# Kernel tuning notes

Hardware: AMD Instinct MI355X
Metric: run time of the kernel (lower is better)

The kernel has to match this reference:

```python
import jax, jax.numpy as jnp
import numpy as np

N, E = 50000, 800000
F_IN, HID, HEADS, NCLS, EF = 16, 32, 4, 5, 8
HC = HID * HEADS
NEG_SLOPE = 0.2


def segment_softmax(scores, seg, num_segments):
    # scores: [E,H], seg: [E] destination node ids
    m = jax.ops.segment_max(scores, seg, num_segments=num_segments)
    e = jnp.exp(scores - m[seg])
    s = jax.ops.segment_sum(e, seg, num_segments=num_segments)
    return e / (s[seg] + 1e-16)


def gat_conv(x, edge_index, edge_attr, W, We, att_src, att_dst, att_edge, bias):
    # PyG GATConv, concat=True, edge_dim=HEADS, eval mode (no dropout)
    n = x.shape[0]
    src, dst = edge_index[0], edge_index[1]
    xp = (x @ W.T).reshape(n, HEADS, HID)                 # [N,H,C]
    a_src = jnp.einsum('nhc,hc->nh', xp, att_src)          # [N,H]
    a_dst = jnp.einsum('nhc,hc->nh', xp, att_dst)
    ep = (edge_attr @ We.T).reshape(-1, HEADS, HID)        # [E,H,C]
    a_e = jnp.einsum('ehc,hc->eh', ep, att_edge)
    alpha = jax.nn.leaky_relu(a_src[src] + a_dst[dst] + a_e, NEG_SLOPE)
    alpha = segment_softmax(alpha, dst, n)                 # softmax over in-edges of dst
    out = jax.ops.segment_sum(xp[src] * alpha[:, :, None], dst, num_segments=n)
    return out.reshape(n, HC) + bias


def setup_inputs() -> dict:
    key = jax.random.key(0)
    ks = jax.random.split(key, 24)
    p = lambda k, shp: (jax.random.normal(k, shp, dtype=jnp.float32) * 0.1)
    inp = {
        'x': jax.random.normal(ks[0], (N, F_IN), dtype=jnp.float32),
        'edge_index': jax.random.randint(ks[1], (2, E), 0, N, dtype=jnp.int64),
        'edge_attr': jax.random.normal(ks[2], (E, EF), dtype=jnp.float32),
        # edge encoder: Linear(EF,HID) -> relu -> Linear(HID,HEADS)
        'ee_w1': p(ks[3], (HID, EF)), 'ee_b1': jnp.zeros((HID,), jnp.float32),
        'ee_w2': p(ks[4], (HEADS, HID)), 'ee_b2': jnp.zeros((HEADS,), jnp.float32),
        # GATConv 1: in=F_IN
        'g1_W': p(ks[5], (HC, F_IN)), 'g1_We': p(ks[6], (HC, HEADS)),
        'g1_as': p(ks[7], (HEADS, HID)), 'g1_ad': p(ks[8], (HEADS, HID)),
        'g1_ae': p(ks[9], (HEADS, HID)), 'g1_b': jnp.zeros((HC,), jnp.float32),
        # GATConv 2: in=HC
        'g2_W': p(ks[10], (HC, HC)), 'g2_We': p(ks[11], (HC, HEADS)),
        'g2_as': p(ks[12], (HEADS, HID)), 'g2_ad': p(ks[13], (HEADS, HID)),
        'g2_ae': p(ks[14], (HEADS, HID)), 'g2_b': jnp.zeros((HC,), jnp.float32),
        # skip projection and classifier
        'skip_w': p(ks[15], (HC, F_IN)), 'skip_b': jnp.zeros((HC,), jnp.float32),
        'cls_w': p(ks[16], (NCLS, HC)), 'cls_b': jnp.zeros((NCLS,), jnp.float32),
    }
    return inp


def reference(x, edge_index, edge_attr, ee_w1, ee_b1, ee_w2, ee_b2,
              g1_W, g1_We, g1_as, g1_ad, g1_ae, g1_b,
              g2_W, g2_We, g2_as, g2_ad, g2_ae, g2_b,
              skip_w, skip_b, cls_w, cls_b):
    ea = jax.nn.relu(edge_attr @ ee_w1.T + ee_b1) @ ee_w2.T + ee_b2   # [E,HEADS]
    skip = x @ skip_w.T + skip_b                                       # [N,HC]
    h = jax.nn.elu(gat_conv(x, edge_index, ea, g1_W, g1_We, g1_as, g1_ad, g1_ae, g1_b))
    h = jax.nn.elu(gat_conv(h, edge_index, ea, g2_W, g2_We, g2_as, g2_ad, g2_ae, g2_b))
    h = h + skip
    return h @ cls_w.T + cls_b                                          # logits [N,NCLS]
```

## Files before the change

### kernel.cpp

```cpp
#include <hip/hip_runtime.h>
#include <hip/hip_bf16.h>
#include <math.h>

#define NN 50000
#define EE 800000
#define F_IN 16
#define HID 32
#define HEADS 4
#define HC 128
#define NCLS 5
#define EF 8
#define NEG_SLOPE 0.2f
#define SCAN_BLOCKS 196
#define NB_NODE 1024
#define NB_EDGE (EE/256)
#define POISON 0xAAAAAAAAu

typedef __attribute__((ext_vector_type(8))) short short8;
typedef __attribute__((ext_vector_type(4))) float floatx4;
typedef __attribute__((ext_vector_type(2))) float floatx2;

__device__ __forceinline__ float lrelu_f(float v) { return v > 0.f ? v : NEG_SLOPE * v; }
__device__ __forceinline__ float elu_f(float v) { return v > 0.f ? v : expm1f(v); }
__device__ __forceinline__ floatx2 splat2(float v) { floatx2 r; r.x = v; r.y = v; return r; }
__device__ __forceinline__ unsigned short f2bf(float v) {
  __hip_bfloat16 b = __float2bfloat16(v);
  unsigned short u; __builtin_memcpy(&u, &b, 2); return u;
}
__device__ __forceinline__ float bf2f(unsigned short u) {
  unsigned v = (unsigned)u << 16; float f; __builtin_memcpy(&f, &v, 4); return f;
}
__device__ __forceinline__ unsigned short pk2_fp8(float a, float b) {
  return (unsigned short)__builtin_amdgcn_cvt_pk_fp8_f32(a, b, 0, false);
}
__device__ __forceinline__ unsigned char pk1_fp8(float a) {
  return (unsigned char)__builtin_amdgcn_cvt_pk_fp8_f32(a, a, 0, false);
}
__device__ __forceinline__ floatx2 unpk_fp8(unsigned short u) {
  return __builtin_amdgcn_cvt_pk_f32_fp8((unsigned)u, false);
}
__device__ __forceinline__ int pk4_fp8(float a, float b, float c, float d) {
  int w = __builtin_amdgcn_cvt_pk_fp8_f32(a, b, 0, false);
  w = __builtin_amdgcn_cvt_pk_fp8_f32(c, d, w, true);
  return w;
}
__device__ __forceinline__ int pk2bf(float a, float b) {
  return (int)((unsigned)f2bf(a) | ((unsigned)f2bf(b) << 16));
}

__global__ void __launch_bounds__(256) k_hist(const int* __restrict__ ei, int* __restrict__ counts,
                                              int* __restrict__ rank) {
  int e = blockIdx.x*256 + threadIdx.x;
  if (e >= EE) return;
  unsigned ret = (unsigned)atomicAdd(&counts[ei[EE + e]], 1);
  rank[e] = (int)(ret - POISON);
}

__global__ void __launch_bounds__(256) k_scan_block(const int* __restrict__ counts, int* __restrict__ bsum) {
  __shared__ int s[256];
  int tid = threadIdx.x;
  int idx = blockIdx.x*256 + tid;
  s[tid] = (idx < NN) ? (int)((unsigned)counts[idx] - POISON) : 0;
  for (int o = 128; o; o >>= 1) { __syncthreads(); if (tid < o) s[tid] += s[tid + o]; }
  if (tid == 0) bsum[blockIdx.x] = s[0];
}

__global__ void __launch_bounds__(256) k_scan_top(const int* __restrict__ bsum, int* __restrict__ bexcl,
                                                  int* __restrict__ row_start,
                                                  const float* __restrict__ clw, const float* __restrict__ skw,
                                                  const float* __restrict__ skb, const float* __restrict__ clb,
                                                  const float* __restrict__ We1, const float* __restrict__ ae1,
                                                  const float* __restrict__ We2, const float* __restrict__ ae2,
                                                  float* __restrict__ mcls, float* __restrict__ cb2,
                                                  float* __restrict__ sve_g) {
  __shared__ int s[256];
  int tid = threadIdx.x;
  int v = (tid < SCAN_BLOCKS) ? bsum[tid] : 0;
  s[tid] = v; __syncthreads();
  for (int o = 1; o < 256; o <<= 1) {
    int t2 = (tid >= o) ? s[tid - o] : 0;
    __syncthreads();
    s[tid] += t2;
    __syncthreads();
  }
  if (tid < SCAN_BLOCKS) bexcl[tid] = s[tid] - v;
  if (tid == 0) row_start[NN] = EE;
  if (tid < NCLS*F_IN) {
    int k = tid >> 4, f = tid & 15;
    float acc = 0.f;
    for (int c = 0; c < HC; ++c) acc = fmaf(clw[k*HC + c], skw[c*F_IN + f], acc);
    mcls[tid] = acc;
  } else if (tid < NCLS*F_IN + NCLS) {
    int k = tid - NCLS*F_IN;
    float acc = clb[k];
    for (int c = 0; c < HC; ++c) acc = fmaf(clw[k*HC + c], skb[c], acc);
    cb2[k] = acc;
  } else if (tid < NCLS*F_IN + NCLS + 32) {
    int t2 = tid - (NCLS*F_IN + NCLS);
    int layer = t2 >> 4, idx = t2 & 15, k = idx >> 2, h = idx & 3;
    const float* We = layer ? We2 : We1;
    const float* ae = layer ? ae2 : ae1;
    float s2 = 0.f;
    for (int c = 0; c < HID; ++c) s2 += We[(h*HID + c)*HEADS + k] * ae[h*HID + c];
    sve_g[layer*16 + k*4 + h] = s2;
  }
}

__global__ void __launch_bounds__(256) k_scan_final(const int* __restrict__ counts, const int* __restrict__ bexcl,
                                                    int* __restrict__ row_start) {
  __shared__ int s[256];
  int tid = threadIdx.x;
  int idx = blockIdx.x*256 + tid;
  int v = (idx < NN) ? (int)((unsigned)counts[idx] - POISON) : 0;
  s[tid] = v; __syncthreads();
  for (int o = 1; o < 256; o <<= 1) {
    int t2 = (tid >= o) ? s[tid - o] : 0;
    __syncthreads();
    s[tid] += t2;
    __syncthreads();
  }
  int excl = s[tid] - v + bexcl[blockIdx.x];
  if (idx < NN) row_start[idx] = excl;
}

__global__ void __launch_bounds__(256) k_fused(
    const float* __restrict__ x, const float* __restrict__ W,
    const float* __restrict__ as_, const float* __restrict__ ad_,
    const float* __restrict__ g2w, unsigned short* __restrict__ w2b,
    unsigned short* __restrict__ xp8u, float* __restrict__ a_src, float* __restrict__ a_dst,
    const float* __restrict__ eattr, const float* __restrict__ w1, const float* __restrict__ b1,
    const float* __restrict__ w2, const float* __restrict__ b2,
    const float* __restrict__ sve_g,
    const int* __restrict__ ei, const int* __restrict__ rank, const int* __restrict__ row_start,
    int4* __restrict__ erec) {
  int tid = threadIdx.x;
  if (blockIdx.x < NB_NODE) {
    __shared__ float sW[HC*17];
    __shared__ float sas[HC], sad[HC];
    __shared__ float sxw[4][16];
    int nb = blockIdx.x;
    if (nb < (HC*HC)/256) w2b[nb*256 + tid] = f2bf(g2w[nb*256 + tid]);
    for (int i = tid; i < HC*F_IN; i += 256) { int r = i >> 4, k = i & 15; sW[r*17 + k] = W[i]; }
    if (tid < HC) { sas[tid] = as_[tid]; sad[tid] = ad_[tid]; }
    __syncthreads();
    int wv = tid >> 6, lane = tid & 63;
    for (int base = nb*4; base < NN; base += NB_NODE*4) {
      int n = base + wv;
      if (n >= NN) continue;
      if (lane < 16) sxw[wv][lane] = x[(size_t)n*F_IN + lane];
      float xv0 = 0.f, xv1 = 0.f;
      #pragma unroll
      for (int k = 0; k < F_IN; ++k) {
        float xk = sxw[wv][k];
        xv0 = fmaf(xk, sW[lane*17 + k], xv0);
        xv1 = fmaf(xk, sW[(lane + 64)*17 + k], xv1);
      }
      float xo0 = __shfl_xor(xv0, 1), xo1 = __shfl_xor(xv1, 1);
      if (!(lane & 1)) {
        xp8u[(size_t)n*64 + (lane >> 1)]      = pk2_fp8(xv0, xo0);
        xp8u[(size_t)n*64 + 32 + (lane >> 1)] = pk2_fp8(xv1, xo1);
      }
      float vs0 = xv0 * sas[lane],      vd0 = xv0 * sad[lane];
      float vs1 = xv1 * sas[lane + 64], vd1 = xv1 * sad[lane + 64];
      #pragma unroll
      for (int m = 16; m; m >>= 1) {
        vs0 += __shfl_xor(vs0, m); vd0 += __shfl_xor(vd0, m);
        vs1 += __shfl_xor(vs1, m); vd1 += __shfl_xor(vd1, m);
      }
      if ((lane & 31) == 0) {
        int hh = lane >> 5;
        a_src[n*HEADS + hh]     = vs0; a_dst[n*HEADS + hh]     = vd0;
        a_src[n*HEADS + 2 + hh] = vs1; a_dst[n*HEADS + 2 + hh] = vd1;
      }
    }
    return;
  }
  int e = (blockIdx.x - NB_NODE)*256 + tid;
  if (e >= EE) return;
  int src = ei[e], dst = ei[EE + e];
  int pos = row_start[dst] + rank[e];
  const float4* ap = (const float4*)(eattr + (size_t)e*EF);
  float4 A0 = ap[0], A1 = ap[1];
  float ea0=A0.x, ea1=A0.y, ea2=A0.z, ea3=A0.w, ea4=A1.x, ea5=A1.y, ea6=A1.z, ea7=A1.w;
  float enc0=b2[0], enc1=b2[1], enc2=b2[2], enc3=b2[3];
  #pragma unroll
  for (int j = 0; j < HID; ++j) {
    float hsum = b1[j];
    hsum = fmaf(ea0, w1[j*EF+0], hsum); hsum = fmaf(ea1, w1[j*EF+1], hsum);
    hsum = fmaf(ea2, w1[j*EF+2], hsum); hsum = fmaf(ea3, w1[j*EF+3], hsum);
    hsum = fmaf(ea4, w1[j*EF+4], hsum); hsum = fmaf(ea5, w1[j*EF+5], hsum);
    hsum = fmaf(ea6, w1[j*EF+6], hsum); hsum = fmaf(ea7, w1[j*EF+7], hsum);
    hsum = fmaxf(hsum, 0.f);
    enc0 = fmaf(hsum, w2[0*HID+j], enc0);
    enc1 = fmaf(hsum, w2[1*HID+j], enc1);
    enc2 = fmaf(hsum, w2[2*HID+j], enc2);
    enc3 = fmaf(hsum, w2[3*HID+j], enc3);
  }
  float ae1_0 = enc0*sve_g[0]  + enc1*sve_g[4]  + enc2*sve_g[8]   + enc3*sve_g[12];
  float ae1_1 = enc0*sve_g[1]  + enc1*sve_g[5]  + enc2*sve_g[9]   + enc3*sve_g[13];
  float ae1_2 = enc0*sve_g[2]  + enc1*sve_g[6]  + enc2*sve_g[10]  + enc3*sve_g[14];
  float ae1_3 = enc0*sve_g[3]  + enc1*sve_g[7]  + enc2*sve_g[11]  + enc3*sve_g[15];
  float ae2_0 = enc0*sve_g[16] + enc1*sve_g[20] + enc2*sve_g[24]  + enc3*sve_g[28];
  float ae2_1 = enc0*sve_g[17] + enc1*sve_g[21] + enc2*sve_g[25]  + enc3*sve_g[29];
  float ae2_2 = enc0*sve_g[18] + enc1*sve_g[22] + enc2*sve_g[26]  + enc3*sve_g[30];
  float ae2_3 = enc0*sve_g[19] + enc1*sve_g[23] + enc2*sve_g[27]  + enc3*sve_g[31];
  int4 r;
  r.x = src;
  r.y = pk2bf(ae1_0, ae1_1);
  r.z = pk2bf(ae1_2, ae1_3);
  r.w = pk4_fp8(ae2_0, ae2_1, ae2_2, ae2_3);
  erec[pos] = r;
}

__global__ void __launch_bounds__(256) k_agg1xp2(
    const int* __restrict__ row_start, const int4* __restrict__ erec,
    const unsigned short* __restrict__ xp8u,
    const float4* __restrict__ a_srcv, const float4* __restrict__ a_dstv,
    const float* __restrict__ bias,
    const unsigned short* __restrict__ w2b,
    const float* __restrict__ as2, const float* __restrict__ ad2,
    unsigned char* __restrict__ xp8u2, float* __restrict__ a_src2, float* __restrict__ a_dst2) {
  __shared__ float4 sew[4][64];
  __shared__ unsigned short h1s[16][136];
  int wv = threadIdx.x >> 6, lane = threadIdx.x & 63;
  int h = lane >> 4, c2 = lane*2;
  for (int i = 0; i < 4; ++i) {
    int n = blockIdx.x*16 + wv*4 + i;
    int beg = row_start[n], end = row_start[n+1];
    float4 ad4 = a_dstv[n];
    floatx2 accA = {0.f, 0.f}, accB = {0.f, 0.f};
    float ssum = 0.f;
    for (int cb = beg; cb < end; cb += 64) {
      int cnt = end - cb; if (cnt > 64) cnt = 64;
      int le = lane < cnt ? lane : cnt - 1;
      int4 rc = erec[cb + le];
      int sl = rc.x;
      float4 as4 = a_srcv[sl];
      float ae0 = bf2f((unsigned short)((unsigned)rc.y & 0xffffu));
      float ae1 = bf2f((unsigned short)((unsigned)rc.y >> 16));
      float ae2 = bf2f((unsigned short)((unsigned)rc.z & 0xffffu));
      float ae3 = bf2f((unsigned short)((unsigned)rc.z >> 16));
      float4 wf;
      wf.x = __expf(lrelu_f(as4.x + ad4.x + ae0));
      wf.y = __expf(lrelu_f(as4.y + ad4.y + ae1));
      wf.z = __expf(lrelu_f(as4.z + ad4.z + ae2));
      wf.w = __expf(lrelu_f(as4.w + ad4.w + ae3));
      if (lane >= cnt) { wf.x = 0.f; wf.y = 0.f; wf.z = 0.f; wf.w = 0.f; }
      sew[wv][lane] = wf;
      const float* ewp = (const float*)(&sew[wv][0]);
      int ng = (cnt + 7) >> 3;
      for (int g = 0; g < ng; ++g) {
        int j8 = g << 3;
        int s0 = __builtin_amdgcn_readlane(sl, j8);
        int s1 = __builtin_amdgcn_readlane(sl, j8+1);
        int s2 = __builtin_amdgcn_readlane(sl, j8+2);
        int s3 = __builtin_amdgcn_readlane(sl, j8+3);
        int s4 = __builtin_amdgcn_readlane(sl, j8+4);
        int s5 = __builtin_amdgcn_readlane(sl, j8+5);
        int s6 = __builtin_amdgcn_readlane(sl, j8+6);
        int s7 = __builtin_amdgcn_readlane(sl, j8+7);
        unsigned short g0 = xp8u[(size_t)s0*64 + lane];
        unsigned short g1 = xp8u[(size_t)s1*64 + lane];
        unsigned short g2 = xp8u[(size_t)s2*64 + lane];
        unsigned short g3 = xp8u[(size_t)s3*64 + lane];
        unsigned short g4 = xp8u[(size_t)s4*64 + lane];
        unsigned short g5 = xp8u[(size_t)s5*64 + lane];
        unsigned short g6 = xp8u[(size_t)s6*64 + lane];
        unsigned short g7 = xp8u[(size_t)s7*64 + lane];
        float w0 = ewp[(j8  )*4 + h], w1 = ewp[(j8+1)*4 + h];
        float w2 = ewp[(j8+2)*4 + h], w3 = ewp[(j8+3)*4 + h];
        float w4 = ewp[(j8+4)*4 + h], w5 = ewp[(j8+5)*4 + h];
        float w6 = ewp[(j8+6)*4 + h], w7 = ewp[(j8+7)*4 + h];
        floatx2 x0 = unpk_fp8(g0), x1 = unpk_fp8(g1), x2 = unpk_fp8(g2), x3 = unpk_fp8(g3);
        floatx2 x4 = unpk_fp8(g4), x5 = unpk_fp8(g5), x6 = unpk_fp8(g6), x7 = unpk_fp8(g7);
        ssum += ((w0 + w1) + (w2 + w3)) + ((w4 + w5) + (w6 + w7));
        accA = __builtin_elementwise_fma(x0, splat2(w0), accA);
        accB = __builtin_elementwise_fma(x1, splat2(w1), accB);
        accA = __builtin_elementwise_fma(x2, splat2(w2), accA);
        accB = __builtin_elementwise_fma(x3, splat2(w3), accB);
        accA = __builtin_elementwise_fma(x4, splat2(w4), accA);
        accB = __builtin_elementwise_fma(x5, splat2(w5), accB);
        accA = __builtin_elementwise_fma(x6, splat2(w6), accA);
        accB = __builtin_elementwise_fma(x7, splat2(w7), accB);
      }
    }
    floatx2 acc = accA + accB;
    float inv = 1.f / (ssum + 1e-16f);
    ushort2 o;
    o.x = f2bf(elu_f(acc.x*inv + bias[c2]));
    o.y = f2bf(elu_f(acc.y*inv + bias[c2+1]));
    *(ushort2*)&h1s[wv*4 + i][c2] = o;
  }
  __syncthreads();
  int ln = lane & 15, quad = lane >> 4;
  int m0 = blockIdx.x*16;
  short8 a[4];
  #pragma unroll
  for (int kc = 0; kc < 4; ++kc)
    a[kc] = *(const short8*)&h1s[ln][(kc*4 + quad)*8];
  float sp[4] = {0.f,0.f,0.f,0.f}, dp[4] = {0.f,0.f,0.f,0.f};
  #pragma unroll
  for (int sub = 0; sub < 2; ++sub) {
    int n0 = wv*2 + sub;
    const short8* brow = (const short8*)(w2b + (size_t)(n0*16 + ln)*HC) + quad;
    floatx4 acc = {0.f, 0.f, 0.f, 0.f};
    #pragma unroll
    for (int kc = 0; kc < 4; ++kc) {
      short8 b = brow[kc*4];
      acc = __builtin_amdgcn_mfma_f32_16x16x32_bf16(a[kc], b, acc, 0, 0, 0);
    }
    float a_sv = as2[wv*HID + sub*16 + ln];
    float a_dv = ad2[wv*HID + sub*16 + ln];
    #pragma unroll
    for (int r = 0; r < 4; ++r) {
      float v = acc[r];
      xp8u2[(size_t)(m0 + quad*4 + r)*HC + n0*16 + ln] = pk1_fp8(v);
      sp[r] = fmaf(v, a_sv, sp[r]);
      dp[r] = fmaf(v, a_dv, dp[r]);
    }
  }
  #pragma unroll
  for (int r = 0; r < 4; ++r) {
    #pragma unroll
    for (int m = 1; m < 16; m <<= 1) {
      sp[r] += __shfl_xor(sp[r], m);
      dp[r] += __shfl_xor(dp[r], m);
    }
  }
  if (ln == 0) {
    #pragma unroll
    for (int r = 0; r < 4; ++r) {
      a_src2[(size_t)(m0 + quad*4 + r)*HEADS + wv] = sp[r];
      a_dst2[(size_t)(m0 + quad*4 + r)*HEADS + wv] = dp[r];
    }
  }
}

#define GROUP8(slv, ewpv, accP, accQ, ssv)                                        \
  {                                                                               \
    int s0_ = __builtin_amdgcn_readlane(slv, j8);                                 \
    int s1_ = __builtin_amdgcn_readlane(slv, j8+1);                               \
    int s2_ = __builtin_amdgcn_readlane(slv, j8+2);                               \
    int s3_ = __builtin_amdgcn_readlane(slv, j8+3);                               \
    int s4_ = __builtin_amdgcn_readlane(slv, j8+4);                               \
    int s5_ = __builtin_amdgcn_readlane(slv, j8+5);                               \
    int s6_ = __builtin_amdgcn_readlane(slv, j8+6);                               \
    int s7_ = __builtin_amdgcn_readlane(slv, j8+7);                               \
    unsigned short g0_ = xp8u2[(size_t)s0_*64 + lane];                            \
    unsigned short g1_ = xp8u2[(size_t)s1_*64 + lane];                            \
    unsigned short g2_ = xp8u2[(size_t)s2_*64 + lane];                            \
    unsigned short g3_ = xp8u2[(size_t)s3_*64 + lane];                            \
    unsigned short g4_ = xp8u2[(size_t)s4_*64 + lane];                            \
    unsigned short g5_ = xp8u2[(size_t)s5_*64 + lane];                            \
    unsigned short g6_ = xp8u2[(size_t)s6_*64 + lane];                            \
    unsigned short g7_ = xp8u2[(size_t)s7_*64 + lane];                            \
    float w0_ = ewpv[(j8  )*4 + h], w1_ = ewpv[(j8+1)*4 + h];                     \
    float w2_ = ewpv[(j8+2)*4 + h], w3_ = ewpv[(j8+3)*4 + h];                     \
    float w4_ = ewpv[(j8+4)*4 + h], w5_ = ewpv[(j8+5)*4 + h];                     \
    float w6_ = ewpv[(j8+6)*4 + h], w7_ = ewpv[(j8+7)*4 + h];                     \
    floatx2 x0_ = unpk_fp8(g0_), x1_ = unpk_fp8(g1_);                             \
    floatx2 x2_ = unpk_fp8(g2_), x3_ = unpk_fp8(g3_);                             \
    floatx2 x4_ = unpk_fp8(g4_), x5_ = unpk_fp8(g5_);                             \
    floatx2 x6_ = unpk_fp8(g6_), x7_ = unpk_fp8(g7_);                             \
    ssv += ((w0_ + w1_) + (w2_ + w3_)) + ((w4_ + w5_) + (w6_ + w7_));             \
    accP = __builtin_elementwise_fma(x0_, splat2(w0_), accP);                     \
    accQ = __builtin_elementwise_fma(x1_, splat2(w1_), accQ);                     \
    accP = __builtin_elementwise_fma(x2_, splat2(w2_), accP);                     \
    accQ = __builtin_elementwise_fma(x3_, splat2(w3_), accQ);                     \
    accP = __builtin_elementwise_fma(x4_, splat2(w4_), accP);                     \
    accQ = __builtin_elementwise_fma(x5_, splat2(w5_), accQ);                     \
    accP = __builtin_elementwise_fma(x6_, splat2(w6_), accP);                     \
    accQ = __builtin_elementwise_fma(x7_, splat2(w7_), accQ);                     \
  }

__global__ void __launch_bounds__(256) k_final(const int* __restrict__ row_start, const int4* __restrict__ erec,
                                               const unsigned short* __restrict__ xp8u2,
                                               const float4* __restrict__ a_srcv, const float4* __restrict__ a_dstv,
                                               const float* __restrict__ g2b, const float* __restrict__ x,
                                               const float* __restrict__ clw, const float* __restrict__ mcls,
                                               const float* __restrict__ cb2,
                                               float* __restrict__ out) {
  __shared__ float4 sew[4][2][64];
  int wv = threadIdx.x >> 6, lane = threadIdx.x & 63;
  int nA = blockIdx.x*8 + wv*2;
  int nB = nA + 1;
  if (nA >= NN) return;
  int h = lane >> 4, c2 = lane*2;
  int begA = row_start[nA], endA = row_start[nA+1];
  int begB = row_start[nB], endB = row_start[nB+1];
  float4 ad4A = a_dstv[nA], ad4B = a_dstv[nB];
  floatx2 accA0 = {0.f,0.f}, accA1 = {0.f,0.f}, accB0 = {0.f,0.f}, accB1 = {0.f,0.f};
  float ssumA = 0.f, ssumB = 0.f;
  int remA = endA - begA, remB = endB - begB;
  int cbA = begA, cbB = begB;
  const float* ewpA = (const float*)(&sew[wv][0][0]);
  const float* ewpB = (const float*)(&sew[wv][1][0]);
  while (remA > 0 || remB > 0) {
    int cntA = remA > 64 ? 64 : (remA > 0 ? remA : 0);
    int cntB = remB > 64 ? 64 : (remB > 0 ? remB : 0);
    int4 rcA, rcB;
    int slA = 0, slB = 0;
    if (cntA > 0) { int le = lane < cntA ? lane : cntA - 1; rcA = erec[cbA + le]; }
    if (cntB > 0) { int le = lane < cntB ? lane : cntB - 1; rcB = erec[cbB + le]; }
    if (cntA > 0) {
      slA = rcA.x;
      float4 as4 = a_srcv[slA];
      floatx2 aelo = __builtin_amdgcn_cvt_pk_f32_fp8((unsigned)rcA.w, false);
      floatx2 aehi = __builtin_amdgcn_cvt_pk_f32_fp8((unsigned)rcA.w, true);
      float4 wf;
      wf.x = __expf(lrelu_f(as4.x + ad4A.x + aelo.x));
      wf.y = __expf(lrelu_f(as4.y + ad4A.y + aelo.y));
      wf.z = __expf(lrelu_f(as4.z + ad4A.z + aehi.x));
      wf.w = __expf(lrelu_f(as4.w + ad4A.w + aehi.y));
      if (lane >= cntA) { wf.x = 0.f; wf.y = 0.f; wf.z = 0.f; wf.w = 0.f; }
      sew[wv][0][lane] = wf;
    } else {
      float4 z = {0.f, 0.f, 0.f, 0.f};
      sew[wv][0][lane] = z;
    }
    if (cntB > 0) {
      slB = rcB.x;
      float4 as4 = a_srcv[slB];
      floatx2 aelo = __builtin_amdgcn_cvt_pk_f32_fp8((unsigned)rcB.w, false);
      floatx2 aehi = __builtin_amdgcn_cvt_pk_f32_fp8((unsigned)rcB.w, true);
      float4 wf;
      wf.x = __expf(lrelu_f(as4.x + ad4B.x + aelo.x));
      wf.y = __expf(lrelu_f(as4.y + ad4B.y + aelo.y));
      wf.z = __expf(lrelu_f(as4.z + ad4B.z + aehi.x));
      wf.w = __expf(lrelu_f(as4.w + ad4B.w + aehi.y));
      if (lane >= cntB) { wf.x = 0.f; wf.y = 0.f; wf.z = 0.f; wf.w = 0.f; }
      sew[wv][1][lane] = wf;
    } else {
      float4 z = {0.f, 0.f, 0.f, 0.f};
      sew[wv][1][lane] = z;
    }
    int cntMax = cntA > cntB ? cntA : cntB;
    int ngMax = (cntMax + 7) >> 3;
    for (int g = 0; g < ngMax; ++g) {
      int j8 = g << 3;
      GROUP8(slA, ewpA, accA0, accA1, ssumA);
      GROUP8(slB, ewpB, accB0, accB1, ssumB);
    }
    cbA += 64; cbB += 64; remA -= 64; remB -= 64;
  }
  floatx2 accA = accA0 + accA1;
  floatx2 accB = accB0 + accB1;
  float invA = 1.f / (ssumA + 1e-16f);
  float invB = 1.f / (ssumB + 1e-16f);
  float b0 = g2b[c2], b1 = g2b[c2+1];
  float v0A = elu_f(accA.x*invA + b0);
  float v1A = elu_f(accA.y*invA + b1);
  float v0B = elu_f(accB.x*invB + b0);
  float v1B = elu_f(accB.y*invB + b1);
  float xvA = x[(size_t)nA*F_IN + (lane & 15)];
  float xvB = x[(size_t)nB*F_IN + (lane & 15)];
  #pragma unroll
  for (int k = 0; k < NCLS; ++k) {
    float2 cw = ((const float2*)(clw + (size_t)k*HC))[lane];
    float pA = fmaf(v0A, cw.x, v1A*cw.y);
    float pB = fmaf(v0B, cw.x, v1B*cw.y);
    if (lane < F_IN) {
      float mk = mcls[k*F_IN + lane];
      pA = fmaf(xvA, mk, pA);
      pB = fmaf(xvB, mk, pB);
    }
    #pragma unroll
    for (int m = 32; m; m >>= 1) {
      pA += __shfl_xor(pA, m);
      pB += __shfl_xor(pB, m);
    }
    if (lane == 0) {
      float ck = cb2[k];
      out[(size_t)nA*NCLS + k] = pA + ck;
      out[(size_t)nB*NCLS + k] = pB + ck;
    }
  }
}

extern "C" void kernel_launch(void* const* d_in, const int* in_sizes, int n_in,
                              void* d_out, int out_size, void* d_ws, size_t ws_size,
                              hipStream_t stream) {
  const float* x      = (const float*)d_in[0];
  const int*   ei     = (const int*)d_in[1];
  const float* eattr  = (const float*)d_in[2];
  const float* ee_w1  = (const float*)d_in[3];
  const float* ee_b1  = (const float*)d_in[4];
  const float* ee_w2  = (const float*)d_in[5];
  const float* ee_b2  = (const float*)d_in[6];
  const float* g1_W   = (const float*)d_in[7];
  const float* g1_We  = (const float*)d_in[8];
  const float* g1_as  = (const float*)d_in[9];
  const float* g1_ad  = (const float*)d_in[10];
  const float* g1_ae  = (const float*)d_in[11];
  const float* g1_b   = (const float*)d_in[12];
  const float* g2_W   = (const float*)d_in[13];
  const float* g2_We  = (const float*)d_in[14];
  const float* g2_as  = (const float*)d_in[15];
  const float* g2_ad  = (const float*)d_in[16];
  const float* g2_ae  = (const float*)d_in[17];
  const float* g2_b   = (const float*)d_in[18];
  const float* skip_w = (const float*)d_in[19];
  const float* skip_b = (const float*)d_in[20];
  const float* cls_w  = (const float*)d_in[21];
  const float* cls_b  = (const float*)d_in[22];
  float* out = (float*)d_out;
  (void)in_sizes; (void)n_in; (void)out_size; (void)ws_size;

  char* ws = (char*)d_ws;
  size_t off = 0;
  auto alloc = [&](size_t bytes) -> void* {
    void* p = ws + off;
    off = (off + bytes + 255) & ~(size_t)255;
    return p;
  };
  int* counts           = (int*)alloc((size_t)NN*4);
  int* row_start        = (int*)alloc((size_t)(NN + 1)*4);
  int* rank             = (int*)alloc((size_t)EE*4);
  int* bexcl            = (int*)alloc(256*4);
  int* bsum             = (int*)alloc(256*4);
  int4* erec            = (int4*)alloc((size_t)EE*16);
  unsigned short* xp8u  = (unsigned short*)alloc((size_t)NN*64*2);
  unsigned char* xp8u2  = (unsigned char*)alloc((size_t)NN*HC);
  unsigned short* w2b   = (unsigned short*)alloc((size_t)HC*HC*2);
  float* a_src          = (float*)alloc((size_t)NN*HEADS*4);
  float* a_dst          = (float*)alloc((size_t)NN*HEADS*4);
  float* a_src2         = (float*)alloc((size_t)NN*HEADS*4);
  float* a_dst2         = (float*)alloc((size_t)NN*HEADS*4);
  float* mcls           = (float*)alloc((size_t)NCLS*F_IN*4);
  float* cb2            = (float*)alloc((size_t)NCLS*4);
  float* sve_g          = (float*)alloc(32*4);

  k_hist<<<EE/256, 256, 0, stream>>>(ei, counts, rank);
  k_scan_block<<<SCAN_BLOCKS, 256, 0, stream>>>(counts, bsum);
  k_scan_top<<<1, 256, 0, stream>>>(bsum, bexcl, row_start, cls_w, skip_w, skip_b, cls_b,
                                    g1_We, g1_ae, g2_We, g2_ae, mcls, cb2, sve_g);
  k_scan_final<<<SCAN_BLOCKS, 256, 0, stream>>>(counts, bexcl, row_start);
  k_fused<<<NB_NODE + NB_EDGE, 256, 0, stream>>>(
      x, g1_W, g1_as, g1_ad, g2_W, w2b, xp8u, a_src, a_dst,
      eattr, ee_w1, ee_b1, ee_w2, ee_b2, sve_g,
      ei, rank, row_start, erec);
  k_agg1xp2<<<NN/16, 256, 0, stream>>>(row_start, erec, xp8u,
                                       (const float4*)a_src, (const float4*)a_dst, g1_b,
                                       w2b, g2_as, g2_ad, xp8u2, a_src2, a_dst2);
  k_final<<<NN/8, 256, 0, stream>>>(row_start, erec, (const unsigned short*)xp8u2,
                                    (const float4*)a_src2, (const float4*)a_dst2,
                                    g2_b, x, cls_w, mcls, cb2, out);
}
```

Before: 285.8 us.

## Merge scan-top into scan-block via last-block flag, replace rank with cursor atomics

Folds the single-block top-level scan into the block-sum kernel using a threadfence plus done-counter so that the last block finishes the scan, removing one kernel launch. The per-edge rank array written by the histogram is replaced by a second atomic counter per destination taken in the edge kernel, saving an E-sized write and read at the cost of extra atomics. The final aggregation kernel stores edge weights per head in a transposed shared layout so each lane reads 8 weights with two float4 loads instead of eight strided scalar loads. Both new counters rely on the workspace starting out filled with the poison pattern.

```diff
diff --git a/kernel.cpp b/kernel.cpp
--- a/kernel.cpp
+++ b/kernel.cpp
@@ -48,34 +48,38 @@
   return (int)((unsigned)f2bf(a) | ((unsigned)f2bf(b) << 16));
 }
 
-__global__ void __launch_bounds__(256) k_hist(const int* __restrict__ ei, int* __restrict__ counts,
-                                              int* __restrict__ rank) {
+__global__ void __launch_bounds__(256) k_hist(const int* __restrict__ ei, int* __restrict__ counts) {
   int e = blockIdx.x*256 + threadIdx.x;
   if (e >= EE) return;
-  unsigned ret = (unsigned)atomicAdd(&counts[ei[EE + e]], 1);
-  rank[e] = (int)(ret - POISON);
-}
-
-__global__ void __launch_bounds__(256) k_scan_block(const int* __restrict__ counts, int* __restrict__ bsum) {
+  atomicAdd(&counts[ei[EE + e]], 1);
+}
+
+__global__ void __launch_bounds__(256) k_scan_block(const int* __restrict__ counts, int* __restrict__ bsum,
+                                                    int* __restrict__ done, int* __restrict__ bexcl,
+                                                    int* __restrict__ row_start,
+                                                    const float* __restrict__ clw, const float* __restrict__ skw,
+                                                    const float* __restrict__ skb, const float* __restrict__ clb,
+                                                    const float* __restrict__ We1, const float* __restrict__ ae1,
+                                                    const float* __restrict__ We2, const float* __restrict__ ae2,
+                                                    float* __restrict__ mcls, float* __restrict__ cb2,
+                                                    float* __restrict__ sve_g) {
   __shared__ int s[256];
+  __shared__ int lastFlag;
   int tid = threadIdx.x;
   int idx = blockIdx.x*256 + tid;
   s[tid] = (idx < NN) ? (int)((unsigned)counts[idx] - POISON) : 0;
   for (int o = 128; o; o >>= 1) { __syncthreads(); if (tid < o) s[tid] += s[tid + o]; }
-  if (tid == 0) bsum[blockIdx.x] = s[0];
-}
-
-__global__ void __launch_bounds__(256) k_scan_top(const int* __restrict__ bsum, int* __restrict__ bexcl,
-                                                  int* __restrict__ row_start,
-                                                  const float* __restrict__ clw, const float* __restrict__ skw,
-                                                  const float* __restrict__ skb, const float* __restrict__ clb,
-                                                  const float* __restrict__ We1, const float* __restrict__ ae1,
-                                                  const float* __restrict__ We2, const float* __restrict__ ae2,
-                                                  float* __restrict__ mcls, float* __restrict__ cb2,
-                                                  float* __restrict__ sve_g) {
-  __shared__ int s[256];
-  int tid = threadIdx.x;
+  if (tid == 0) {
+    bsum[blockIdx.x] = s[0];
+    __threadfence();
+    unsigned old = (unsigned)atomicAdd(done, 1);
+    lastFlag = ((old - POISON) == (unsigned)(SCAN_BLOCKS - 1)) ? 1 : 0;
+  }
+  __syncthreads();
+  if (!lastFlag) return;
+  __threadfence();
   int v = (tid < SCAN_BLOCKS) ? bsum[tid] : 0;
+  __syncthreads();
   s[tid] = v; __syncthreads();
   for (int o = 1; o < 256; o <<= 1) {
     int t2 = (tid >= o) ? s[tid - o] : 0;
@@ -97,7 +101,7 @@
     cb2[k] = acc;
   } else if (tid < NCLS*F_IN + NCLS + 32) {
     int t2 = tid - (NCLS*F_IN + NCLS);
-    int layer = t2 >> 4, idx = t2 & 15, k = idx >> 2, h = idx & 3;
+    int layer = t2 >> 4, idx2 = t2 & 15, k = idx2 >> 2, h = idx2 & 3;
     const float* We = layer ? We2 : We1;
     const float* ae = layer ? ae2 : ae1;
     float s2 = 0.f;
@@ -131,7 +135,7 @@
     const float* __restrict__ eattr, const float* __restrict__ w1, const float* __restrict__ b1,
     const float* __restrict__ w2, const float* __restrict__ b2,
     const float* __restrict__ sve_g,
-    const int* __restrict__ ei, const int* __restrict__ rank, const int* __restrict__ row_start,
+    const int* __restrict__ ei, int* __restrict__ cursor, const int* __restrict__ row_start,
     int4* __restrict__ erec) {
   int tid = threadIdx.x;
   if (blockIdx.x < NB_NODE) {
@@ -178,7 +182,7 @@
   int e = (blockIdx.x - NB_NODE)*256 + tid;
   if (e >= EE) return;
   int src = ei[e], dst = ei[EE + e];
-  int pos = row_start[dst] + rank[e];
+  int pos = row_start[dst] + (int)((unsigned)atomicAdd(&cursor[dst], 1) - POISON);
   const float4* ap = (const float4*)(eattr + (size_t)e*EF);
   float4 A0 = ap[0], A1 = ap[1];
   float ea0=A0.x, ea1=A0.y, ea2=A0.z, ea3=A0.w, ea4=A1.x, ea5=A1.y, ea6=A1.z, ea7=A1.w;
@@ -336,7 +340,7 @@
   }
 }
 
-#define GROUP8(slv, ewpv, accP, accQ, ssv)                                        \
+#define GROUP8(slv, wrowv, accP, accQ, ssv)                                       \
   {                                                                               \
     int s0_ = __builtin_amdgcn_readlane(slv, j8);                                 \
     int s1_ = __builtin_amdgcn_readlane(slv, j8+1);                               \
@@ -354,10 +358,10 @@
     unsigned short g5_ = xp8u2[(size_t)s5_*64 + lane];                            \
     unsigned short g6_ = xp8u2[(size_t)s6_*64 + lane];                            \
     unsigned short g7_ = xp8u2[(size_t)s7_*64 + lane];                            \
-    float w0_ = ewpv[(j8  )*4 + h], w1_ = ewpv[(j8+1)*4 + h];                     \
-    float w2_ = ewpv[(j8+2)*4 + h], w3_ = ewpv[(j8+3)*4 + h];                     \
-    float w4_ = ewpv[(j8+4)*4 + h], w5_ = ewpv[(j8+5)*4 + h];                     \
-    float w6_ = ewpv[(j8+6)*4 + h], w7_ = ewpv[(j8+7)*4 + h];                     \
+    float4 wlo_ = *(const float4*)&wrowv[j8];                                     \
+    float4 whi_ = *(const float4*)&wrowv[j8+4];                                   \
+    float w0_ = wlo_.x, w1_ = wlo_.y, w2_ = wlo_.z, w3_ = wlo_.w;                 \
+    float w4_ = whi_.x, w5_ = whi_.y, w6_ = whi_.z, w7_ = whi_.w;                 \
     floatx2 x0_ = unpk_fp8(g0_), x1_ = unpk_fp8(g1_);                             \
     floatx2 x2_ = unpk_fp8(g2_), x3_ = unpk_fp8(g3_);                             \
     floatx2 x4_ = unpk_fp8(g4_), x5_ = unpk_fp8(g5_);                             \
@@ -380,7 +384,7 @@
                                                const float* __restrict__ clw, const float* __restrict__ mcls,
                                                const float* __restrict__ cb2,
                                                float* __restrict__ out) {
-  __shared__ float4 sew[4][2][64];
+  __shared__ float sewT[4][2][4][68];
   int wv = threadIdx.x >> 6, lane = threadIdx.x & 63;
   int nA = blockIdx.x*8 + wv*2;
   int nB = nA + 1;
@@ -393,8 +397,8 @@
   float ssumA = 0.f, ssumB = 0.f;
   int remA = endA - begA, remB = endB - begB;
   int cbA = begA, cbB = begB;
-  const float* ewpA = (const float*)(&sew[wv][0][0]);
-  const float* ewpB = (const float*)(&sew[wv][1][0]);
+  const float* wrA = &sewT[wv][0][h][0];
+  const float* wrB = &sewT[wv][1][h][0];
   while (remA > 0 || remB > 0) {
     int cntA = remA > 64 ? 64 : (remA > 0 ? remA : 0);
     int cntB = remB > 64 ? 64 : (remB > 0 ? remB : 0);
@@ -413,10 +417,15 @@
       wf.z = __expf(lrelu_f(as4.z + ad4A.z + aehi.x));
       wf.w = __expf(lrelu_f(as4.w + ad4A.w + aehi.y));
       if (lane >= cntA) { wf.x = 0.f; wf.y = 0.f; wf.z = 0.f; wf.w = 0.f; }
-      sew[wv][0][lane] = wf;
+      sewT[wv][0][0][lane] = wf.x;
+      sewT[wv][0][1][lane] = wf.y;
+      sewT[wv][0][2][lane] = wf.z;
+      sewT[wv][0][3][lane] = wf.w;
     } else {
-      float4 z = {0.f, 0.f, 0.f, 0.f};
-      sew[wv][0][lane] = z;
+      sewT[wv][0][0][lane] = 0.f;
+      sewT[wv][0][1][lane] = 0.f;
+      sewT[wv][0][2][lane] = 0.f;
+      sewT[wv][0][3][lane] = 0.f;
     }
     if (cntB > 0) {
       slB = rcB.x;
@@ -429,17 +438,22 @@
       wf.z = __expf(lrelu_f(as4.z + ad4B.z + aehi.x));
       wf.w = __expf(lrelu_f(as4.w + ad4B.w + aehi.y));
       if (lane >= cntB) { wf.x = 0.f; wf.y = 0.f; wf.z = 0.f; wf.w = 0.f; }
-      sew[wv][1][lane] = wf;
+      sewT[wv][1][0][lane] = wf.x;
+      sewT[wv][1][1][lane] = wf.y;
+      sewT[wv][1][2][lane] = wf.z;
+      sewT[wv][1][3][lane] = wf.w;
     } else {
-      float4 z = {0.f, 0.f, 0.f, 0.f};
-      sew[wv][1][lane] = z;
+      sewT[wv][1][0][lane] = 0.f;
+      sewT[wv][1][1][lane] = 0.f;
+      sewT[wv][1][2][lane] = 0.f;
+      sewT[wv][1][3][lane] = 0.f;
     }
     int cntMax = cntA > cntB ? cntA : cntB;
     int ngMax = (cntMax + 7) >> 3;
     for (int g = 0; g < ngMax; ++g) {
       int j8 = g << 3;
-      GROUP8(slA, ewpA, accA0, accA1, ssumA);
-      GROUP8(slB, ewpB, accB0, accB1, ssumB);
+      GROUP8(slA, wrA, accA0, accA1, ssumA);
+      GROUP8(slB, wrB, accB0, accB1, ssumB);
     }
     cbA += 64; cbB += 64; remA -= 64; remB -= 64;
   }
@@ -515,9 +529,10 @@
   };
   int* counts           = (int*)alloc((size_t)NN*4);
   int* row_start        = (int*)alloc((size_t)(NN + 1)*4);
-  int* rank             = (int*)alloc((size_t)EE*4);
+  int* cursor           = (int*)alloc((size_t)NN*4);
   int* bexcl            = (int*)alloc(256*4);
   int* bsum             = (int*)alloc(256*4);
+  int* done             = (int*)alloc(256*4);
   int4* erec            = (int4*)alloc((size_t)EE*16);
   unsigned short* xp8u  = (unsigned short*)alloc((size_t)NN*64*2);
   unsigned char* xp8u2  = (unsigned char*)alloc((size_t)NN*HC);
@@ -530,15 +545,15 @@
   float* cb2            = (float*)alloc((size_t)NCLS*4);
   float* sve_g          = (float*)alloc(32*4);
 
-  k_hist<<<EE/256, 256, 0, stream>>>(ei, counts, rank);
-  k_scan_block<<<SCAN_BLOCKS, 256, 0, stream>>>(counts, bsum);
-  k_scan_top<<<1, 256, 0, stream>>>(bsum, bexcl, row_start, cls_w, skip_w, skip_b, cls_b,
-                                    g1_We, g1_ae, g2_We, g2_ae, mcls, cb2, sve_g);
+  k_hist<<<EE/256, 256, 0, stream>>>(ei, counts);
+  k_scan_block<<<SCAN_BLOCKS, 256, 0, stream>>>(counts, bsum, done, bexcl, row_start,
+                                                cls_w, skip_w, skip_b, cls_b,
+                                                g1_We, g1_ae, g2_We, g2_ae, mcls, cb2, sve_g);
   k_scan_final<<<SCAN_BLOCKS, 256, 0, stream>>>(counts, bexcl, row_start);
   k_fused<<<NB_NODE + NB_EDGE, 256, 0, stream>>>(
       x, g1_W, g1_as, g1_ad, g2_W, w2b, xp8u, a_src, a_dst,
       eattr, ee_w1, ee_b1, ee_w2, ee_b2, sve_g,
-      ei, rank, row_start, erec);
+      ei, cursor, row_start, erec);
   k_agg1xp2<<<NN/16, 256, 0, stream>>>(row_start, erec, xp8u,
                                        (const float4*)a_src, (const float4*)a_dst, g1_b,
                                        w2b, g2_as, g2_ad, xp8u2, a_src2, a_dst2);
```

New measurement: 303.3 us. +6.1%, slower.
